# Kernel optimization log

Hardware: AMD Instinct MI355X
Metric: run time of the kernel (lower is better)

Reference implementation:

```python
import jax, jax.numpy as jnp
import numpy as np

N = 100000   # nodes
E = 1600000  # edges
IN, H1, H2, OUT = 128, 256, 128, 16


def setup_inputs() -> dict:
    key = jax.random.key(0)
    ks = jax.random.split(key, 20)

    def lin(kw, fan_in, fan_out):
        s = 1.0 / np.sqrt(fan_in)
        return jax.random.uniform(kw, (fan_in, fan_out), jnp.float32, -s, s)

    inp = {
        "x": jax.random.normal(ks[0], (N, IN), jnp.float32),
        "edge_index": jax.random.randint(ks[1], (2, E), 0, N, jnp.int64),
        # main branch
        "W1": lin(ks[2], IN, H1), "b1": jnp.zeros((H1,), jnp.float32),
        "W2": lin(ks[3], H1, H2), "b2": jnp.zeros((H2,), jnp.float32),
        "Wc": lin(ks[4], H2, OUT), "bc": jnp.zeros((OUT,), jnp.float32),
        # encoder branch (4 GCN layers)
        "We1": lin(ks[5], IN, H2), "be1": jnp.zeros((H2,), jnp.float32),
        "We2": lin(ks[6], H2, H2), "be2": jnp.zeros((H2,), jnp.float32),
        "We3": lin(ks[7], H2, H2), "be3": jnp.zeros((H2,), jnp.float32),
        "We4": lin(ks[8], H2, H2), "be4": jnp.zeros((H2,), jnp.float32),
        # trustworthiness head
        "Wt": lin(ks[9], H2, 2), "bt": jnp.zeros((2,), jnp.float32),
    }
    return inp


def _gcn(x, W, b, row, col, dis):
    # PyG GCNConv: out = D^-1/2 (A + I) D^-1/2 (x W) + b
    xw = x @ W                                   # [N, F]
    norm = dis[row] * dis[col]                   # [E]
    msg = xw[row] * norm[:, None]                # [E, F]  (gather + scale)
    agg = jax.ops.segment_sum(msg, col, num_segments=N)
    agg = agg + xw * (dis * dis)[:, None]        # self-loop contribution
    return agg + b


def reference(x, edge_index, W1, b1, W2, b2, Wc, bc,
              We1, be1, We2, be2, We3, be3, We4, be4, Wt, bt):
    row, col = edge_index[0], edge_index[1]
    # degree with self-loops, shared across all conv layers (same graph)
    deg = jax.ops.segment_sum(jnp.ones((E,), x.dtype), col, num_segments=N) + 1.0
    dis = deg ** -0.5

    # classification branch
    h = jax.nn.relu(_gcn(x, W1, b1, row, col, dis))
    h = _gcn(h, W2, b2, row, col, dis)
    class_logits = h @ Wc + bc

    # encoder branch -> trust head
    h2 = _gcn(x, We1, be1, row, col, dis)
    h2 = _gcn(h2, We2, be2, row, col, dis)
    h2 = _gcn(h2, We3, be3, row, col, dis)
    h2 = _gcn(h2, We4, be4, row, col, dis)
    trust_prob = jax.nn.sigmoid(h2 @ Wt + bt)

    return (class_logits, trust_prob)
```

## Files before the change

kernel.cpp:

```cpp
#include <hip/hip_runtime.h>
#include <math.h>


#define SM_W2C   0
#define SM_T4    4096
#define SM_T3    4352
#define SM_T2    4608
#define SM_ME    4864
#define SM_CLSC  5120
#define SM_C1    5136
#define SM_C2    5138
#define SM_C3    5140
#define SM_FC    5142
#define SM_TOTAL 5248

typedef __attribute__((ext_vector_type(8))) short bf16x8;
typedef __attribute__((ext_vector_type(4))) float f32x4;
#define MFMA16(a, b, c) __builtin_amdgcn_mfma_f32_16x16x32_bf16(a, b, c, 0, 0, 0)

__device__ inline unsigned short f2bf(float f) {
  unsigned u = __float_as_uint(f);
  u += 0x7fffu + ((u >> 16) & 1u);
  return (unsigned short)(u >> 16);
}
__device__ inline float bf2f(unsigned short h) {
  return __uint_as_float((unsigned)h << 16);
}

__global__ __launch_bounds__(256) void k_deg(const int* __restrict__ ei,
                                             int* __restrict__ deg, int E, int N) {
  int e = blockIdx.x * 256 + threadIdx.x;
  if (e < E) {
    unsigned c = (unsigned)ei[E + e];
    if (c >= (unsigned)N) c = 0;
    atomicAdd(&deg[c], 1);
  }
}

__global__ __launch_bounds__(256) void k_dis(const int* __restrict__ deg,
                                             float* __restrict__ dis, int N) {
  int i = blockIdx.x * 256 + threadIdx.x;
  if (i < N) dis[i] = 1.0f / sqrtf((float)deg[i] + 1.0f);
}

__global__ __launch_bounds__(1024) void k_scan(const int* __restrict__ cnt,
                                               int* __restrict__ rowptr, int n) {
  __shared__ int wsum[16];
  __shared__ int s_carry;
  int tid = threadIdx.x, lane = tid & 63, wid = tid >> 6;
  if (tid == 0) { s_carry = 0; rowptr[0] = 0; }
  __syncthreads();
  for (int base = 0; base < n; base += 1024) {
    int i = base + tid;
    int v = (i < n) ? cnt[i] : 0;
    int x = v;
    #pragma unroll
    for (int off = 1; off < 64; off <<= 1) {
      int t = __shfl_up(x, off, 64);
      if (lane >= off) x += t;
    }
    if (lane == 63) wsum[wid] = x;
    __syncthreads();
    if (wid == 0 && lane < 16) {
      int ws = wsum[lane];
      #pragma unroll
      for (int off = 1; off < 16; off <<= 1) {
        int t = __shfl_up(ws, off, 64);
        if (lane >= off) ws += t;
      }
      wsum[lane] = ws;
    }
    __syncthreads();
    int incl = x + (wid ? wsum[wid - 1] : 0);
    int carry = s_carry;
    if (i < n) rowptr[i + 1] = carry + incl;
    __syncthreads();
    if (tid == 1023) s_carry = carry + incl;
    __syncthreads();
  }
}

__global__ __launch_bounds__(256) void k_scatter(const int* __restrict__ ei,
                                                 const int* __restrict__ rowptr,
                                                 int* __restrict__ cnt,
                                                 const float* __restrict__ dis,
                                                 int* __restrict__ csr_src,
                                                 float* __restrict__ csr_w,
                                                 int E, int N) {
  int e = blockIdx.x * 256 + threadIdx.x;
  if (e >= E) return;
  unsigned r = (unsigned)ei[e];
  unsigned c = (unsigned)ei[E + e];
  if (r >= (unsigned)N) r = 0;
  if (c >= (unsigned)N) c = 0;
  int pos = rowptr[c] + atomicAdd(&cnt[c], 1);
  csr_src[pos] = (int)r;
  csr_w[pos] = dis[r] * dis[c];
}

__global__ __launch_bounds__(256) void k_precompute(
    const float* __restrict__ W1,
    const float* __restrict__ W2, const float* __restrict__ b2,
    const float* __restrict__ Wc, const float* __restrict__ bc,
    const float* __restrict__ We1, const float* __restrict__ be1,
    const float* __restrict__ We2, const float* __restrict__ be2,
    const float* __restrict__ We3, const float* __restrict__ be3,
    const float* __restrict__ We4, const float* __restrict__ be4,
    const float* __restrict__ Wt, const float* __restrict__ bt,
    float* __restrict__ sm,
    unsigned short* __restrict__ w1h, unsigned short* __restrict__ w1l,
    unsigned short* __restrict__ w2h, unsigned short* __restrict__ w2l) {
  int tid = threadIdx.x;
  {
    int r = tid >> 1, c = tid & 1; float s = 0.f;
    for (int k = 0; k < 128; ++k) s += We4[r * 128 + k] * Wt[k * 2 + c];
    sm[SM_T4 + r * 2 + c] = s;
  }
  __syncthreads();
  {
    int r = tid >> 1, c = tid & 1; float s = 0.f;
    for (int k = 0; k < 128; ++k) s += We3[r * 128 + k] * sm[SM_T4 + k * 2 + c];
    sm[SM_T3 + r * 2 + c] = s;
  }
  __syncthreads();
  {
    int r = tid >> 1, c = tid & 1; float s = 0.f;
    for (int k = 0; k < 128; ++k) s += We2[r * 128 + k] * sm[SM_T3 + k * 2 + c];
    sm[SM_T2 + r * 2 + c] = s;
  }
  __syncthreads();
  {
    int r = tid >> 1, c = tid & 1; float s = 0.f;
    for (int k = 0; k < 128; ++k) s += We1[r * 128 + k] * sm[SM_T2 + k * 2 + c];
    sm[SM_ME + r * 2 + c] = s;
  }
  for (int o = tid; o < 4096; o += 256) {
    int r = o >> 4, c = o & 15; float s = 0.f;
    for (int k = 0; k < 128; ++k) s += W2[r * 128 + k] * Wc[k * 16 + c];
    sm[SM_W2C + o] = s;
  }
  if (tid < 16) {
    float s = 0.f;
    for (int k = 0; k < 128; ++k) s += b2[k] * Wc[k * 16 + tid];
    sm[SM_CLSC + tid] = s + bc[tid];
  }
  __syncthreads();
  if (tid < 2) {
    float s = 0.f;
    for (int k = 0; k < 128; ++k) s += be1[k] * sm[SM_T2 + k * 2 + tid];
    sm[SM_C1 + tid] = s;
    s = 0.f;
    for (int k = 0; k < 128; ++k) s += be2[k] * sm[SM_T3 + k * 2 + tid];
    sm[SM_C2 + tid] = s;
    s = 0.f;
    for (int k = 0; k < 128; ++k) s += be3[k] * sm[SM_T4 + k * 2 + tid];
    sm[SM_C3 + tid] = s;
    s = 0.f;
    for (int k = 0; k < 128; ++k) s += be4[k] * Wt[k * 2 + tid];
    sm[SM_FC + tid] = s + bt[tid];
  }
  for (int idx = tid; idx < 32768; idx += 256) {
    int c = idx >> 7, k = idx & 127;
    float v = W1[(size_t)k * 256 + c];
    unsigned short h = f2bf(v);
    w1h[idx] = h;
    w1l[idx] = f2bf(v - bf2f(h));
  }
  for (int idx = tid; idx < 4096; idx += 256) {
    int c = idx >> 8, k = idx & 255;
    float v = sm[SM_W2C + k * 16 + c];
    unsigned short h = f2bf(v);
    w2h[idx] = h;
    w2l[idx] = f2bf(v - bf2f(h));
  }
}

__global__ __launch_bounds__(256) void k_agg128(
    const float* __restrict__ x, const int* __restrict__ rowptr,
    const int* __restrict__ csr_src, const float* __restrict__ csr_w,
    const float* __restrict__ dis, const float* __restrict__ sm,
    unsigned short* __restrict__ axh, unsigned short* __restrict__ axl,
    float* __restrict__ ga, int N) {
  int node = blockIdx.x * 4 + (threadIdx.x >> 6);
  if (node >= N) return;
  int lane = threadIdx.x & 63;
  const float2* x2 = (const float2*)x;
  float d = dis[node];
  float2 v = x2[(size_t)node * 64 + lane];
  float a0 = d * d * v.x, a1 = d * d * v.y;
  int e = rowptr[node], end = rowptr[node + 1];
  while (e < end) {
    int rem = end - e;
    int cnt = rem < 64 ? rem : 64;
    int off = lane < cnt ? lane : cnt - 1;
    int src_l = csr_src[e + off];
    int w_l = __float_as_int(csr_w[e + off]);
    for (int i = 0; i < cnt; ++i) {
      int s = __builtin_amdgcn_readlane(src_l, i);
      float w = __int_as_float(__builtin_amdgcn_readlane(w_l, i));
      float2 u = x2[(size_t)s * 64 + lane];
      a0 = fmaf(w, u.x, a0);
      a1 = fmaf(w, u.y, a1);
    }
    e += 64;
  }
  unsigned short h0 = f2bf(a0), h1v = f2bf(a1);
  unsigned short l0 = f2bf(a0 - bf2f(h0)), l1 = f2bf(a1 - bf2f(h1v));
  ((unsigned int*)axh)[(size_t)node * 64 + lane] = (unsigned)h0 | ((unsigned)h1v << 16);
  ((unsigned int*)axl)[(size_t)node * 64 + lane] = (unsigned)l0 | ((unsigned)l1 << 16);
  float4 me = *(const float4*)&sm[SM_ME + lane * 4];
  float p0 = a0 * me.x + a1 * me.z;
  float p1 = a0 * me.y + a1 * me.w;
  #pragma unroll
  for (int m = 32; m; m >>= 1) { p0 += __shfl_xor(p0, m); p1 += __shfl_xor(p1, m); }
  if (lane == 0)
    ((float2*)ga)[node] = make_float2(p0 + sm[SM_C1 + 0], p1 + sm[SM_C1 + 1]);
}

__global__ __launch_bounds__(256, 2) void k_gemm_mfma(
    const unsigned short* __restrict__ axh, const unsigned short* __restrict__ axl,
    const unsigned short* __restrict__ w1h, const unsigned short* __restrict__ w1l,
    const unsigned short* __restrict__ w2h, const unsigned short* __restrict__ w2l,
    const float* __restrict__ b1, float* __restrict__ Y, int N) {
  __shared__ unsigned short lds[32768];
  int tid = threadIdx.x, lane = tid & 63, w = tid >> 6;
  int r16 = lane & 15, kh = lane >> 4;
  int m0 = blockIdx.x * 64;
  #pragma unroll
  for (int it = 0; it < 8; ++it) {
    int idx = it * 256 + tid;
    int arr = idx >> 10, rem = idx & 1023;
    int row = rem >> 4, ch = rem & 15;
    int gr = m0 + row; if (gr > N - 1) gr = N - 1;
    const unsigned short* src = (arr ? axl : axh) + (size_t)gr * 128 + ch * 8;
    uint4 vv = *(const uint4*)src;
    *(uint4*)&lds[arr * 8192 + row * 128 + ((ch ^ (row & 7)) * 8)] = vv;
  }
  __syncthreads();
  f32x4 acc[4][4];
  #pragma unroll
  for (int i = 0; i < 4; ++i)
    #pragma unroll
    for (int j = 0; j < 4; ++j) acc[i][j] = (f32x4){0.f, 0.f, 0.f, 0.f};
  #pragma unroll
  for (int ks = 0; ks < 4; ++ks) {
    bf16x8 bh[4], bl[4];
    #pragma unroll
    for (int nt = 0; nt < 4; ++nt) {
      int col = w * 64 + nt * 16 + r16;
      size_t boff = (size_t)col * 128 + ks * 32 + kh * 8;
      bh[nt] = *(const bf16x8*)(w1h + boff);
      bl[nt] = *(const bf16x8*)(w1l + boff);
    }
    #pragma unroll
    for (int mt = 0; mt < 4; ++mt) {
      int row = mt * 16 + r16;
      int ch = ks * 4 + kh;
      int off = row * 128 + ((ch ^ (row & 7)) * 8);
      bf16x8 ah = *(const bf16x8*)&lds[off];
      bf16x8 al = *(const bf16x8*)&lds[8192 + off];
      #pragma unroll
      for (int nt = 0; nt < 4; ++nt) {
        acc[mt][nt] = MFMA16(ah, bh[nt], acc[mt][nt]);
        acc[mt][nt] = MFMA16(ah, bl[nt], acc[mt][nt]);
        acc[mt][nt] = MFMA16(al, bh[nt], acc[mt][nt]);
      }
    }
  }
  __syncthreads();
  #pragma unroll
  for (int nt = 0; nt < 4; ++nt) {
    int colL = w * 64 + nt * 16 + r16;
    float bv = b1[colL];
    #pragma unroll
    for (int mt = 0; mt < 4; ++mt) {
      #pragma unroll
      for (int r = 0; r < 4; ++r) {
        int rowL = mt * 16 + kh * 4 + r;
        float vv = acc[mt][nt][r] + bv;
        vv = vv > 0.f ? vv : 0.f;
        unsigned short hh = f2bf(vv);
        unsigned short ll = f2bf(vv - bf2f(hh));
        int idx = rowL * 256 + (colL ^ ((rowL & 7) << 3));
        lds[idx] = hh;
        lds[16384 + idx] = ll;
      }
    }
  }
  __syncthreads();
  f32x4 y = (f32x4){0.f, 0.f, 0.f, 0.f};
  int rowL = w * 16 + r16;
  #pragma unroll
  for (int k2 = 0; k2 < 8; ++k2) {
    int cb = k2 * 32 + kh * 8;
    int idx = rowL * 256 + (cb ^ ((rowL & 7) << 3));
    bf16x8 a2h = *(const bf16x8*)&lds[idx];
    bf16x8 a2l = *(const bf16x8*)&lds[16384 + idx];
    size_t boff = (size_t)r16 * 256 + cb;
    bf16x8 b2h = *(const bf16x8*)(w2h + boff);
    bf16x8 b2l = *(const bf16x8*)(w2l + boff);
    y = MFMA16(a2h, b2h, y);
    y = MFMA16(a2h, b2l, y);
    y = MFMA16(a2l, b2h, y);
  }
  #pragma unroll
  for (int r = 0; r < 4; ++r) {
    int gr = m0 + w * 16 + kh * 4 + r;
    if (gr < N) Y[(size_t)gr * 16 + r16] = y[r];
  }
}

__global__ __launch_bounds__(256) void k_agg16(
    const float* __restrict__ Y, const int* __restrict__ rowptr,
    const int* __restrict__ csr_src, const float* __restrict__ csr_w,
    const float* __restrict__ dis, const float* __restrict__ sm,
    float* __restrict__ out, int N) {
  int node = blockIdx.x * 16 + (threadIdx.x >> 4);
  if (node >= N) return;
  int sl = threadIdx.x & 15;
  float d = dis[node];
  float acc = d * d * Y[(size_t)node * 16 + sl];
  int e = rowptr[node], end = rowptr[node + 1];
  for (; e < end; ++e) {
    int s = csr_src[e]; float w = csr_w[e];
    acc = fmaf(w, Y[(size_t)s * 16 + sl], acc);
  }
  out[(size_t)node * 16 + sl] = acc + sm[SM_CLSC + sl];
}

template <int FINAL>
__global__ __launch_bounds__(256) void k_agg2(
    const float* __restrict__ gin, const int* __restrict__ rowptr,
    const int* __restrict__ csr_src, const float* __restrict__ csr_w,
    const float* __restrict__ dis, const float* __restrict__ cadd,
    float* __restrict__ gout, int N) {
  int i = blockIdx.x * 256 + threadIdx.x;
  if (i >= N) return;
  const float2* g2 = (const float2*)gin;
  float d = dis[i];
  float2 v = g2[i];
  float a0 = d * d * v.x, a1 = d * d * v.y;
  int e = rowptr[i], end = rowptr[i + 1];
  for (; e < end; ++e) {
    int s = csr_src[e]; float w = csr_w[e];
    float2 u = g2[s];
    a0 = fmaf(w, u.x, a0); a1 = fmaf(w, u.y, a1);
  }
  a0 += cadd[0]; a1 += cadd[1];
  if (FINAL) {
    a0 = 1.f / (1.f + expf(-a0));
    a1 = 1.f / (1.f + expf(-a1));
  }
  ((float2*)gout)[i] = make_float2(a0, a1);
}

extern "C" void kernel_launch(void* const* d_in, const int* in_sizes, int n_in,
                              void* d_out, int out_size, void* d_ws, size_t ws_size,
                              hipStream_t stream) {
  const float* x = (const float*)d_in[0];
  const int* ei = (const int*)d_in[1];
  const float* W1 = (const float*)d_in[2];
  const float* b1 = (const float*)d_in[3];
  const float* W2 = (const float*)d_in[4];
  const float* b2 = (const float*)d_in[5];
  const float* Wc = (const float*)d_in[6];
  const float* bc = (const float*)d_in[7];
  const float* We1 = (const float*)d_in[8];
  const float* be1 = (const float*)d_in[9];
  const float* We2 = (const float*)d_in[10];
  const float* be2 = (const float*)d_in[11];
  const float* We3 = (const float*)d_in[12];
  const float* be3 = (const float*)d_in[13];
  const float* We4 = (const float*)d_in[14];
  const float* be4 = (const float*)d_in[15];
  const float* Wt = (const float*)d_in[16];
  const float* bt = (const float*)d_in[17];
  float* out = (float*)d_out;

  const int N = in_sizes[0] / 128;
  const int E = in_sizes[1] / 2;

  char* ws = (char*)d_ws;
  size_t off = 0;
  auto alloc = [&](size_t bytes) {
    size_t o = off;
    off = (off + bytes + 255) & ~(size_t)255;
    return o;
  };
  int* deg = (int*)(ws + alloc((size_t)N * 4));
  int* cnt = (int*)(ws + alloc((size_t)N * 4));
  int* rowptr = (int*)(ws + alloc(((size_t)N + 1) * 4));
  float* dis = (float*)(ws + alloc((size_t)N * 4));
  int* csr_src = (int*)(ws + alloc((size_t)E * 4));
  float* csr_w = (float*)(ws + alloc((size_t)E * 4));
  unsigned short* axh = (unsigned short*)(ws + alloc((size_t)N * 128 * 2));
  unsigned short* axl = (unsigned short*)(ws + alloc((size_t)N * 128 * 2));
  float* y16 = (float*)(ws + alloc((size_t)N * 16 * 4));
  float* ga = (float*)(ws + alloc((size_t)N * 2 * 4));
  float* gb = (float*)(ws + alloc((size_t)N * 2 * 4));
  float* sm = (float*)(ws + alloc((size_t)SM_TOTAL * 4));
  unsigned short* w1h = (unsigned short*)(ws + alloc(32768 * 2));
  unsigned short* w1l = (unsigned short*)(ws + alloc(32768 * 2));
  unsigned short* w2h = (unsigned short*)(ws + alloc(4096 * 2));
  unsigned short* w2l = (unsigned short*)(ws + alloc(4096 * 2));

  hipMemsetAsync(deg, 0, (size_t)N * 4, stream);
  hipMemsetAsync(cnt, 0, (size_t)N * 4, stream);

  k_precompute<<<1, 256, 0, stream>>>(W1, W2, b2, Wc, bc, We1, be1, We2, be2,
                                      We3, be3, We4, be4, Wt, bt, sm,
                                      w1h, w1l, w2h, w2l);
  k_deg<<<(E + 255) / 256, 256, 0, stream>>>(ei, deg, E, N);
  k_dis<<<(N + 255) / 256, 256, 0, stream>>>(deg, dis, N);
  k_scan<<<1, 1024, 0, stream>>>(deg, rowptr, N);
  k_scatter<<<(E + 255) / 256, 256, 0, stream>>>(ei, rowptr, cnt, dis, csr_src,
                                                 csr_w, E, N);
  k_agg128<<<(N + 3) / 4, 256, 0, stream>>>(x, rowptr, csr_src, csr_w, dis, sm,
                                            axh, axl, ga, N);
  k_gemm_mfma<<<(N + 63) / 64, 256, 0, stream>>>(axh, axl, w1h, w1l, w2h, w2l,
                                                 b1, y16, N);
  k_agg16<<<(N + 15) / 16, 256, 0, stream>>>(y16, rowptr, csr_src, csr_w, dis,
                                             sm, out, N);
  k_agg2<0><<<(N + 255) / 256, 256, 0, stream>>>(ga, rowptr, csr_src, csr_w,
                                                 dis, sm + SM_C2, gb, N);
  k_agg2<0><<<(N + 255) / 256, 256, 0, stream>>>(gb, rowptr, csr_src, csr_w,
                                                 dis, sm + SM_C3, ga, N);
  k_agg2<1><<<(N + 255) / 256, 256, 0, stream>>>(
      ga, rowptr, csr_src, csr_w, dis, sm + SM_FC, out + (size_t)N * 16, N);
}
```

Baseline: 725.2 us.

## Parallelize degree scan and weight precompute across multiple blocks

```diff
diff --git a/kernel.cpp b/kernel.cpp
--- a/kernel.cpp
+++ b/kernel.cpp
@@ -37,47 +37,57 @@
   }
 }
 
-__global__ __launch_bounds__(256) void k_dis(const int* __restrict__ deg,
-                                             float* __restrict__ dis, int N) {
+__global__ __launch_bounds__(1024) void k_scan1(const int* __restrict__ deg,
+                                                int* __restrict__ rowptr,
+                                                int* __restrict__ bsum,
+                                                float* __restrict__ dis, int n) {
+  __shared__ int wsum[16];
+  int tid = threadIdx.x, lane = tid & 63, wid = tid >> 6;
+  int i = blockIdx.x * 1024 + tid;
+  int v = (i < n) ? deg[i] : 0;
+  if (i < n) dis[i] = 1.0f / sqrtf((float)v + 1.0f);
+  int x = v;
+  #pragma unroll
+  for (int off = 1; off < 64; off <<= 1) {
+    int t = __shfl_up(x, off, 64);
+    if (lane >= off) x += t;
+  }
+  if (lane == 63) wsum[wid] = x;
+  __syncthreads();
+  if (wid == 0 && lane < 16) {
+    int ws = wsum[lane];
+    #pragma unroll
+    for (int off = 1; off < 16; off <<= 1) {
+      int t = __shfl_up(ws, off, 64);
+      if (lane >= off) ws += t;
+    }
+    wsum[lane] = ws;
+  }
+  __syncthreads();
+  int incl = x + (wid ? wsum[wid - 1] : 0);
+  if (i < n) rowptr[i + 1] = incl;
+  if (tid == 0) bsum[blockIdx.x] = wsum[15];
+}
+
+__global__ __launch_bounds__(128) void k_scan2(int* __restrict__ bsum,
+                                               int* __restrict__ rowptr, int B) {
+  __shared__ int s[128];
+  int tid = threadIdx.x;
+  s[tid] = (tid < B) ? bsum[tid] : 0;
+  __syncthreads();
+  if (tid == 0) {
+    int acc = 0;
+    for (int j = 0; j < B; ++j) { int t = s[j]; s[j] = acc; acc += t; }
+    rowptr[0] = 0;
+  }
+  __syncthreads();
+  if (tid < B) bsum[tid] = s[tid];
+}
+
+__global__ __launch_bounds__(256) void k_scan3(int* __restrict__ rowptr,
+                                               const int* __restrict__ bsum, int n) {
   int i = blockIdx.x * 256 + threadIdx.x;
-  if (i < N) dis[i] = 1.0f / sqrtf((float)deg[i] + 1.0f);
-}
-
-__global__ __launch_bounds__(1024) void k_scan(const int* __restrict__ cnt,
-                                               int* __restrict__ rowptr, int n) {
-  __shared__ int wsum[16];
-  __shared__ int s_carry;
-  int tid = threadIdx.x, lane = tid & 63, wid = tid >> 6;
-  if (tid == 0) { s_carry = 0; rowptr[0] = 0; }
-  __syncthreads();
-  for (int base = 0; base < n; base += 1024) {
-    int i = base + tid;
-    int v = (i < n) ? cnt[i] : 0;
-    int x = v;
-    #pragma unroll
-    for (int off = 1; off < 64; off <<= 1) {
-      int t = __shfl_up(x, off, 64);
-      if (lane >= off) x += t;
-    }
-    if (lane == 63) wsum[wid] = x;
-    __syncthreads();
-    if (wid == 0 && lane < 16) {
-      int ws = wsum[lane];
-      #pragma unroll
-      for (int off = 1; off < 16; off <<= 1) {
-        int t = __shfl_up(ws, off, 64);
-        if (lane >= off) ws += t;
-      }
-      wsum[lane] = ws;
-    }
-    __syncthreads();
-    int incl = x + (wid ? wsum[wid - 1] : 0);
-    int carry = s_carry;
-    if (i < n) rowptr[i + 1] = carry + incl;
-    __syncthreads();
-    if (tid == 1023) s_carry = carry + incl;
-    __syncthreads();
-  }
+  if (i < n) rowptr[i + 1] += bsum[i >> 10];
 }
 
 __global__ __launch_bounds__(256) void k_scatter(const int* __restrict__ ei,
@@ -110,7 +120,31 @@
     float* __restrict__ sm,
     unsigned short* __restrict__ w1h, unsigned short* __restrict__ w1l,
     unsigned short* __restrict__ w2h, unsigned short* __restrict__ w2l) {
-  int tid = threadIdx.x;
+  int tid = threadIdx.x, b = blockIdx.x;
+  if (b < 16) {
+    int r = b * 16 + (tid >> 4), c = tid & 15;
+    float s = 0.f;
+    #pragma unroll 4
+    for (int k = 0; k < 128; ++k) s += W2[(size_t)r * 128 + k] * Wc[k * 16 + c];
+    sm[SM_W2C + r * 16 + c] = s;
+    unsigned short h = f2bf(s);
+    w2h[c * 256 + r] = h;
+    w2l[c * 256 + r] = f2bf(s - bf2f(h));
+    return;
+  }
+  if (b < 32) {
+    int base = (b - 16) * 2048;
+    #pragma unroll
+    for (int it = 0; it < 8; ++it) {
+      int idx = base + it * 256 + tid;
+      int c = idx >> 7, k = idx & 127;
+      float v = W1[(size_t)k * 256 + c];
+      unsigned short h = f2bf(v);
+      w1h[idx] = h;
+      w1l[idx] = f2bf(v - bf2f(h));
+    }
+    return;
+  }
   {
     int r = tid >> 1, c = tid & 1; float s = 0.f;
     for (int k = 0; k < 128; ++k) s += We4[r * 128 + k] * Wt[k * 2 + c];
@@ -133,11 +167,6 @@
     int r = tid >> 1, c = tid & 1; float s = 0.f;
     for (int k = 0; k < 128; ++k) s += We1[r * 128 + k] * sm[SM_T2 + k * 2 + c];
     sm[SM_ME + r * 2 + c] = s;
-  }
-  for (int o = tid; o < 4096; o += 256) {
-    int r = o >> 4, c = o & 15; float s = 0.f;
-    for (int k = 0; k < 128; ++k) s += W2[r * 128 + k] * Wc[k * 16 + c];
-    sm[SM_W2C + o] = s;
   }
   if (tid < 16) {
     float s = 0.f;
@@ -158,20 +187,6 @@
     s = 0.f;
     for (int k = 0; k < 128; ++k) s += be4[k] * Wt[k * 2 + tid];
     sm[SM_FC + tid] = s + bt[tid];
-  }
-  for (int idx = tid; idx < 32768; idx += 256) {
-    int c = idx >> 7, k = idx & 127;
-    float v = W1[(size_t)k * 256 + c];
-    unsigned short h = f2bf(v);
-    w1h[idx] = h;
-    w1l[idx] = f2bf(v - bf2f(h));
-  }
-  for (int idx = tid; idx < 4096; idx += 256) {
-    int c = idx >> 8, k = idx & 255;
-    float v = sm[SM_W2C + k * 16 + c];
-    unsigned short h = f2bf(v);
-    w2h[idx] = h;
-    w2l[idx] = f2bf(v - bf2f(h));
   }
 }
 
@@ -379,6 +394,7 @@
 
   const int N = in_sizes[0] / 128;
   const int E = in_sizes[1] / 2;
+  const int NB = (N + 1023) / 1024;
 
   char* ws = (char*)d_ws;
   size_t off = 0;
@@ -387,9 +403,10 @@
     off = (off + bytes + 255) & ~(size_t)255;
     return o;
   };
-  int* deg = (int*)(ws + alloc((size_t)N * 4));
-  int* cnt = (int*)(ws + alloc((size_t)N * 4));
+  int* deg = (int*)(ws + alloc((size_t)N * 8));
+  int* cnt = deg + N;
   int* rowptr = (int*)(ws + alloc(((size_t)N + 1) * 4));
+  int* bsum = (int*)(ws + alloc(128 * 4));
   float* dis = (float*)(ws + alloc((size_t)N * 4));
   int* csr_src = (int*)(ws + alloc((size_t)E * 4));
   float* csr_w = (float*)(ws + alloc((size_t)E * 4));
@@ -404,15 +421,15 @@
   unsigned short* w2h = (unsigned short*)(ws + alloc(4096 * 2));
   unsigned short* w2l = (unsigned short*)(ws + alloc(4096 * 2));
 
-  hipMemsetAsync(deg, 0, (size_t)N * 4, stream);
-  hipMemsetAsync(cnt, 0, (size_t)N * 4, stream);
-
-  k_precompute<<<1, 256, 0, stream>>>(W1, W2, b2, Wc, bc, We1, be1, We2, be2,
-                                      We3, be3, We4, be4, Wt, bt, sm,
-                                      w1h, w1l, w2h, w2l);
+  hipMemsetAsync(deg, 0, (size_t)N * 8, stream);
+
+  k_precompute<<<33, 256, 0, stream>>>(W1, W2, b2, Wc, bc, We1, be1, We2, be2,
+                                       We3, be3, We4, be4, Wt, bt, sm,
+                                       w1h, w1l, w2h, w2l);
   k_deg<<<(E + 255) / 256, 256, 0, stream>>>(ei, deg, E, N);
-  k_dis<<<(N + 255) / 256, 256, 0, stream>>>(deg, dis, N);
-  k_scan<<<1, 1024, 0, stream>>>(deg, rowptr, N);
+  k_scan1<<<NB, 1024, 0, stream>>>(deg, rowptr, bsum, dis, N);
+  k_scan2<<<1, 128, 0, stream>>>(bsum, rowptr, NB);
+  k_scan3<<<(N + 255) / 256, 256, 0, stream>>>(rowptr, bsum, N);
   k_scatter<<<(E + 255) / 256, 256, 0, stream>>>(ei, rowptr, cnt, dis, csr_src,
                                                  csr_w, E, N);
   k_agg128<<<(N + 3) / 4, 256, 0, stream>>>(x, rowptr, csr_src, csr_w, dis, sm,
```

Result: faster. 582.0 us (-19.8%).
